# Kernel optimization log

Hardware: AMD Instinct MI355X
Metric: run time of the kernel (lower is better)

## Reference

```python
import jax, jax.numpy as jnp
import numpy as np
import math

N_NODES = 100000
N_EDGES = 3200000
F_IN = 512
HID = 128
N_CLS = 16


def setup_inputs() -> dict:
    key = jax.random.key(0)
    k = jax.random.split(key, 6)
    x = jax.random.normal(k[0], (N_NODES, F_IN), dtype=jnp.float32)
    edge_index = jax.random.randint(k[1], (2, N_EDGES), 0, N_NODES, dtype=jnp.int32)
    W1 = jax.random.normal(k[2], (F_IN, HID), dtype=jnp.float32) / np.sqrt(F_IN)
    W2 = jax.random.normal(k[3], (HID, HID), dtype=jnp.float32) / np.sqrt(HID)
    W3 = jax.random.normal(k[4], (N_CLS, HID), dtype=jnp.float32) / np.sqrt(HID)
    b3 = jnp.zeros((N_CLS,), dtype=jnp.float32)
    return {"x": x, "edge_index": edge_index, "W1": W1, "W2": W2, "W3": W3, "b3": b3}


def _sym_norm(edge_index, num_nodes, dtype):
    # add self loops with fill_value = trunc(log2(average_node_degree))
    E = edge_index.shape[1]
    fill = float(math.trunc(math.log2(E / num_nodes)))
    loops = jnp.arange(num_nodes, dtype=edge_index.dtype)
    row = jnp.concatenate([edge_index[0], loops])
    col = jnp.concatenate([edge_index[1], loops])
    w = jnp.concatenate([jnp.ones((E,), dtype), jnp.full((num_nodes,), fill, dtype)])
    deg = jax.ops.segment_sum(w, row, num_segments=num_nodes)
    deg_inv_sqrt = jnp.where(deg > 0, jax.lax.rsqrt(deg), 0.0)
    norm = deg_inv_sqrt[row] * w * deg_inv_sqrt[col]
    return row, col, norm


def reference(x, edge_index, W1, W2, W3, b3):
    N = x.shape[0]
    row, col, norm = _sym_norm(edge_index, N, x.dtype)

    def gcn(h, W):
        h = h @ W                                   # [N, d_out]
        msg = norm[:, None] * h[col]                # gather + scale, [E', d_out]
        return jax.ops.segment_sum(msg, row, num_segments=N)

    h = jax.nn.relu(gcn(x, W1))      # layer 1 + srelu (threshold clamped at 0)
    h = gcn(h, W2)                   # layer 2
    # dropout p=0.5 is identity in eval mode
    return h @ W3.T + b3             # linear classifier [N, n_classes]
```

## Files before the change

### kernel.cpp

```cpp
#include <hip/hip_runtime.h>
#include <cmath>

typedef __attribute__((ext_vector_type(8))) short short8;
typedef __attribute__((ext_vector_type(8))) unsigned short ushort8;
typedef __attribute__((ext_vector_type(4))) float f32x4;
typedef __attribute__((ext_vector_type(2))) float f32x2;
typedef __attribute__((ext_vector_type(4))) unsigned int uint4v;
typedef __attribute__((ext_vector_type(2))) int int2v;

#define EPB 4096
#define BCAP 20480

__device__ inline float bf16_lo(unsigned int p) {
  union { unsigned int i; float f; } v; v.i = p << 16; return v.f;
}
__device__ inline float bf16_hi(unsigned int p) {
  union { unsigned int i; float f; } v; v.i = p & 0xffff0000u; return v.f;
}
__device__ inline f32x2 bf2(unsigned int p) {
  union { unsigned int i; float f; } lo, hi;
  lo.i = p << 16;
  hi.i = p & 0xffff0000u;
  return (f32x2){lo.f, hi.f};
}
__device__ inline float bf16u(unsigned short w) {
  union { unsigned int i; float f; } v; v.i = (unsigned int)w << 16; return v.f;
}
__device__ inline unsigned short f32_to_bf16(float f) {
  union { float f; unsigned int i; } v; v.f = f;
  unsigned int x = v.i;
  x += 0x7fffu + ((x >> 16) & 1u);
  return (unsigned short)(x >> 16);
}

__global__ __launch_bounds__(256) void bin_k(const int* __restrict__ rows,
                                             const int* __restrict__ cols,
                                             int* __restrict__ bucket_cursor,
                                             unsigned int* __restrict__ binned, int E) {
  __shared__ int lhist[256];
  __shared__ int gbase[256];
  __shared__ int loff[256];
  const int t = threadIdx.x;
  const int base = blockIdx.x * EPB;
  lhist[t] = 0;
  __syncthreads();

  int bk[16];
  unsigned int pk[16];
#pragma unroll
  for (int j = 0; j < 16; ++j) {
    int e = base + j * 256 + t;
    if (e < E) {
      int r = rows[e];
      int c = cols[e];
      bk[j] = r >> 9;
      pk[j] = ((unsigned int)(r & 511) << 17) | (unsigned int)c;
      atomicAdd(&lhist[bk[j]], 1);
    } else {
      bk[j] = -1;
    }
  }
  __syncthreads();
  if (lhist[t] > 0) gbase[t] = atomicAdd(&bucket_cursor[t], lhist[t]);
  loff[t] = 0;
  __syncthreads();
#pragma unroll
  for (int j = 0; j < 16; ++j) {
    if (bk[j] >= 0) {
      int rank = gbase[bk[j]] + atomicAdd(&loff[bk[j]], 1);
      if (rank < BCAP) binned[(size_t)bk[j] * BCAP + rank] = pk[j];
    }
  }
}

__global__ __launch_bounds__(1024) void bucket_csr_k(const unsigned int* __restrict__ binned,
                                                     const int* __restrict__ bucket_cursor,
                                                     int2v* __restrict__ rowse,
                                                     float* __restrict__ dis,
                                                     int* __restrict__ col_sorted,
                                                     int N, float fill) {
  __shared__ int lcnt[512];
  __shared__ int lscan[512];
  const int b = blockIdx.x;
  const int t = threadIdx.x;
  const int start = b * BCAP;
  int cnt = bucket_cursor[b];
  if (cnt > BCAP) cnt = BCAP;
  const int endb = start + cnt;
  const int rbase = b << 9;

  if (t < 512) lcnt[t] = 0;
  __syncthreads();
  for (int i = start + t; i < endb; i += 1024)
    atomicAdd(&lcnt[binned[i] >> 17], 1);
  __syncthreads();

  int v = (t < 512) ? lcnt[t] : 0;
  if (t < 512) lscan[t] = v;
  __syncthreads();
  for (int off = 1; off < 512; off <<= 1) {
    int add = (t < 512 && t >= off) ? lscan[t - off] : 0;
    __syncthreads();
    if (t < 512) lscan[t] += add;
    __syncthreads();
  }

  if (t < 512) {
    int excl = lscan[t] - v;
    int r = rbase + t;
    if (r < N) {
      rowse[r] = (int2v){start + excl, start + excl + v};
      float d = (float)v + fill;
      dis[r] = d > 0.f ? rsqrtf(d) : 0.f;
    }
    lcnt[t] = excl;
  }
  __syncthreads();

  for (int i = start + t; i < endb; i += 1024) {
    unsigned int pk = binned[i];
    int rl = (int)(pk >> 17);
    int c = (int)(pk & 0x1FFFFu);
    int pos = atomicAdd(&lcnt[rl], 1);
    col_sorted[start + pos] = c;
  }
}

__global__ __launch_bounds__(256) void cast_w_k(const float* __restrict__ W1,
                                                const float* __restrict__ W2,
                                                const float* __restrict__ W3,
                                                unsigned short* __restrict__ W1t,
                                                unsigned short* __restrict__ W2t,
                                                unsigned short* __restrict__ W3b,
                                                int FIN) {
  int g = blockIdx.x * 256 + threadIdx.x;
  int n1 = FIN * 128;
  if (g < n1) {
    int n = g & 127, k = g >> 7;
    W1t[n * FIN + k] = f32_to_bf16(W1[(size_t)k * 128 + n]);
  } else if (g < n1 + 128 * 128) {
    int gg = g - n1;
    int n = gg & 127, k = gg >> 7;
    W2t[n * 128 + k] = f32_to_bf16(W2[k * 128 + n]);
  } else if (g < n1 + 128 * 128 + 16 * 128) {
    int gg = g - n1 - 128 * 128;
    W3b[gg] = f32_to_bf16(W3[gg]);
  }
}

__global__ __launch_bounds__(256) void gemm_k(const void* __restrict__ Aq, int a_is_f32,
                                              int M, int K,
                                              const unsigned short* __restrict__ Bt,
                                              const float* __restrict__ dis,
                                              unsigned short* __restrict__ C) {
  __shared__ unsigned short Al[64 * 40];
  __shared__ unsigned short Bl[128 * 40];
  const int t = threadIdx.x;
  const int bm = blockIdx.x * 64;
  const int lane = t & 63;
  const int wave = t >> 6;
  const int wm = (wave >> 1) * 32;
  const int wn = (wave & 1) * 64;
  const int l15 = lane & 15;
  const int l4 = lane >> 4;

  f32x4 acc[2][4];
#pragma unroll
  for (int a = 0; a < 2; ++a)
#pragma unroll
    for (int b = 0; b < 4; ++b) acc[a][b] = (f32x4){0.f, 0.f, 0.f, 0.f};

  const int am = t >> 2;
  const int ak = (t & 3) * 8;
  const int bn = t >> 1;
  const int bk = (t & 1) * 16;
  const int arow = bm + am;
  const bool arow_ok = arow < M;

  auto load_a = [&](int k0) -> ushort8 {
    ushort8 av = {0, 0, 0, 0, 0, 0, 0, 0};
    if (a_is_f32) {
      const float* A = (const float*)Aq;
      if (arow_ok) {
        const float* p = A + (size_t)arow * K + k0 + ak;
#pragma unroll
        for (int j = 0; j < 8; ++j) av[j] = f32_to_bf16(p[j]);
      }
    } else {
      const unsigned short* A = (const unsigned short*)Aq;
      if (arow_ok) av = *(const ushort8*)(A + (size_t)arow * K + k0 + ak);
    }
    return av;
  };

  ushort8 av = load_a(0);
  ushort8 bv0 = *(const ushort8*)(Bt + (size_t)bn * K + bk);
  ushort8 bv1 = *(const ushort8*)(Bt + (size_t)bn * K + bk + 8);

  for (int k0 = 0; k0 < K; k0 += 32) {
    *(ushort8*)&Al[am * 40 + ak] = av;
    *(ushort8*)&Bl[bn * 40 + bk] = bv0;
    *(ushort8*)&Bl[bn * 40 + bk + 8] = bv1;
    __syncthreads();

    const int kn = k0 + 32;
    if (kn < K) {
      av = load_a(kn);
      bv0 = *(const ushort8*)(Bt + (size_t)bn * K + kn + bk);
      bv1 = *(const ushort8*)(Bt + (size_t)bn * K + kn + bk + 8);
    }

    short8 a0 = *(const short8*)&Al[(wm + l15) * 40 + l4 * 8];
    short8 a1 = *(const short8*)&Al[(wm + 16 + l15) * 40 + l4 * 8];
#pragma unroll
    for (int nt = 0; nt < 4; ++nt) {
      short8 bfr = *(const short8*)&Bl[(wn + nt * 16 + l15) * 40 + l4 * 8];
      acc[0][nt] = __builtin_amdgcn_mfma_f32_16x16x32_bf16(a0, bfr, acc[0][nt], 0, 0, 0);
      acc[1][nt] = __builtin_amdgcn_mfma_f32_16x16x32_bf16(a1, bfr, acc[1][nt], 0, 0, 0);
    }
    __syncthreads();
  }

#pragma unroll
  for (int mt = 0; mt < 2; ++mt) {
    int rbase = bm + wm + mt * 16 + l4 * 4;
#pragma unroll
    for (int r = 0; r < 4; ++r) {
      int row = rbase + r;
      if (row < M) {
        float dr = dis[row];
#pragma unroll
        for (int nt = 0; nt < 4; ++nt) {
          int col = wn + nt * 16 + l15;
          C[(size_t)row * 128 + col] = f32_to_bf16(acc[mt][nt][r] * dr);
        }
      }
    }
  }
}

__global__ __launch_bounds__(256) void agg_k(const unsigned short* __restrict__ hs,
                                             const int2v* __restrict__ rowse,
                                             const int* __restrict__ cols,
                                             const float* __restrict__ dis,
                                             unsigned short* __restrict__ out_bf,
                                             const unsigned short* __restrict__ W3b,
                                             const float* __restrict__ b3,
                                             float* __restrict__ fcout,
                                             int N, float fill, int mode) {
  int r = blockIdx.x * 4 + (threadIdx.x >> 6);
  if (r >= N) return;
  const int lane = threadIdx.x & 63;
  const int sub = lane >> 4;
  const int fl = lane & 15;
  const uint4v* hv = (const uint4v*)hs;

  f32x2 a4[4];
#pragma unroll
  for (int k = 0; k < 4; ++k) a4[k] = (f32x2){0.f, 0.f};

  int2v se = rowse[r];
  int e = se.x;
  const int end = se.y;

  for (; e + 32 <= end; e += 32) {
    unsigned int c0 = (unsigned int)cols[e + sub];
    unsigned int c1 = (unsigned int)cols[e + 4 + sub];
    unsigned int c2 = (unsigned int)cols[e + 8 + sub];
    unsigned int c3 = (unsigned int)cols[e + 12 + sub];
    unsigned int c4 = (unsigned int)cols[e + 16 + sub];
    unsigned int c5 = (unsigned int)cols[e + 20 + sub];
    unsigned int c6 = (unsigned int)cols[e + 24 + sub];
    unsigned int c7 = (unsigned int)cols[e + 28 + sub];
    uint4v p0 = hv[c0 * 16u + fl];
    uint4v p1 = hv[c1 * 16u + fl];
    uint4v p2 = hv[c2 * 16u + fl];
    uint4v p3 = hv[c3 * 16u + fl];
    uint4v p4 = hv[c4 * 16u + fl];
    uint4v p5 = hv[c5 * 16u + fl];
    uint4v p6 = hv[c6 * 16u + fl];
    uint4v p7 = hv[c7 * 16u + fl];
#pragma unroll
    for (int k = 0; k < 4; ++k) {
      f32x2 s0 = (bf2(p0[k]) + bf2(p1[k])) + (bf2(p2[k]) + bf2(p3[k]));
      f32x2 s1 = (bf2(p4[k]) + bf2(p5[k])) + (bf2(p6[k]) + bf2(p7[k]));
      a4[k] += s0 + s1;
    }
  }
  for (; e + 8 <= end; e += 8) {
    unsigned int c0 = (unsigned int)cols[e + sub];
    unsigned int c1 = (unsigned int)cols[e + 4 + sub];
    uint4v p0 = hv[c0 * 16u + fl];
    uint4v p1 = hv[c1 * 16u + fl];
#pragma unroll
    for (int k = 0; k < 4; ++k) a4[k] += bf2(p0[k]) + bf2(p1[k]);
  }
  for (; e < end; e += 4) {
    int ee = e + sub;
    bool ok = ee < end;
    unsigned int c = ok ? (unsigned int)cols[ee] : (unsigned int)r;
    uint4v p = hv[c * 16u + fl];
    if (!ok) p = (uint4v){0, 0, 0, 0};
#pragma unroll
    for (int k = 0; k < 4; ++k) a4[k] += bf2(p[k]);
  }

#pragma unroll
  for (int k = 0; k < 4; ++k) {
    a4[k].x += __shfl_xor(a4[k].x, 16);
    a4[k].y += __shfl_xor(a4[k].y, 16);
    a4[k].x += __shfl_xor(a4[k].x, 32);
    a4[k].y += __shfl_xor(a4[k].y, 32);
  }

  if (sub == 0) {
    uint4v ps = hv[(unsigned int)r * 16u + fl];
    float dr = dis[r];
    float v[8];
#pragma unroll
    for (int k = 0; k < 4; ++k) {
      v[2 * k]     = dr * (a4[k].x + fill * bf16_lo(ps[k]));
      v[2 * k + 1] = dr * (a4[k].y + fill * bf16_hi(ps[k]));
    }
    if (mode == 0) {
      uint4v o;
#pragma unroll
      for (int k = 0; k < 4; ++k) {
        float f0 = fmaxf(v[2 * k], 0.f);
        float f1 = fmaxf(v[2 * k + 1], 0.f);
        o[k] = ((unsigned int)f32_to_bf16(f1) << 16) | (unsigned int)f32_to_bf16(f0);
      }
      *((uint4v*)out_bf + (unsigned int)r * 16u + fl) = o;
    } else {
      float p[16];
#pragma unroll
      for (int c = 0; c < 16; ++c) {
        ushort8 wr = *(const ushort8*)(W3b + c * 128 + fl * 8);
        float s = v[0] * bf16u(wr[0]);
        s = fmaf(v[1], bf16u(wr[1]), s);
        s = fmaf(v[2], bf16u(wr[2]), s);
        s = fmaf(v[3], bf16u(wr[3]), s);
        s = fmaf(v[4], bf16u(wr[4]), s);
        s = fmaf(v[5], bf16u(wr[5]), s);
        s = fmaf(v[6], bf16u(wr[6]), s);
        s = fmaf(v[7], bf16u(wr[7]), s);
        p[c] = s;
      }
#pragma unroll
      for (int m = 1; m <= 8; m <<= 1)
#pragma unroll
        for (int c = 0; c < 16; ++c) p[c] += __shfl_xor(p[c], m);
      fcout[(size_t)r * 16 + fl] = p[fl] + b3[fl];
    }
  }
}

extern "C" void kernel_launch(void* const* d_in, const int* in_sizes, int n_in,
                              void* d_out, int out_size, void* d_ws, size_t ws_size,
                              hipStream_t stream) {
  const float* x  = (const float*)d_in[0];
  const int* edge = (const int*)d_in[1];
  const float* W1 = (const float*)d_in[2];
  const float* W2 = (const float*)d_in[3];
  const float* W3 = (const float*)d_in[4];
  const float* b3 = (const float*)d_in[5];
  float* out = (float*)d_out;

  const int HID = 128;
  const int FIN = in_sizes[2] / HID;
  const int N   = in_sizes[0] / FIN;
  const int E   = in_sizes[1] / 2;
  const float fill = truncf(log2f((float)E / (float)N));

  char* w = (char*)d_ws;
  size_t off = 0;
  auto alloc = [&](size_t bytes) -> void* {
    void* p = w + off;
    off += (bytes + 255) & ~(size_t)255;
    return p;
  };
  const int NB = (N + 511) >> 9;
  float* dis      = (float*)alloc((size_t)N * 4);
  int2v* rowse    = (int2v*)alloc((size_t)N * 8);
  int* col_sorted = (int*)alloc((size_t)NB * BCAP * 4);
  int* bucket_cursor = (int*)alloc(256 * 4);
  unsigned int* binned = (unsigned int*)alloc((size_t)NB * BCAP * 4);
  unsigned short* W1t  = (unsigned short*)alloc((size_t)FIN * 128 * 2);
  unsigned short* W2t  = (unsigned short*)alloc(128 * 128 * 2);
  unsigned short* W3b  = (unsigned short*)alloc(16 * 128 * 2);
  unsigned short* bufA = (unsigned short*)alloc((size_t)N * 128 * 2);
  unsigned short* bufB = (unsigned short*)alloc((size_t)N * 128 * 2);

  const int* rows  = edge;
  const int* colsp = edge + E;

  hipMemsetAsync(bucket_cursor, 0, 256 * 4, stream);
  bin_k<<<(E + EPB - 1) / EPB, 256, 0, stream>>>(rows, colsp, bucket_cursor, binned, E);
  bucket_csr_k<<<NB, 1024, 0, stream>>>(binned, bucket_cursor, rowse, dis,
                                        col_sorted, N, fill);
  const int castN = FIN * 128 + 128 * 128 + 16 * 128;
  cast_w_k<<<(castN + 255) / 256, 256, 0, stream>>>(W1, W2, W3, W1t, W2t, W3b, FIN);

  const int gm = (N + 63) / 64;
  gemm_k<<<gm, 256, 0, stream>>>(x, 1, N, FIN, W1t, dis, bufA);
  agg_k<<<(N + 3) / 4, 256, 0, stream>>>(bufA, rowse, col_sorted, dis, bufB,
                                         W3b, b3, out, N, fill, 0);
  gemm_k<<<gm, 256, 0, stream>>>(bufB, 0, N, HID, W2t, dis, bufA);
  agg_k<<<(N + 3) / 4, 256, 0, stream>>>(bufA, rowse, col_sorted, dis, bufB,
                                         W3b, b3, out, N, fill, 1);
}
```

Baseline: 651.6 us.

## Map one 16-lane group per row with degree-sorted row permutation in aggregation

```diff
diff --git a/kernel.cpp b/kernel.cpp
--- a/kernel.cpp
+++ b/kernel.cpp
@@ -31,6 +31,11 @@
   unsigned int x = v.i;
   x += 0x7fffu + ((x >> 16) & 1u);
   return (unsigned short)(x >> 16);
+}
+__device__ inline f32x2 pk_add(f32x2 a, f32x2 b) {
+  f32x2 d;
+  asm("v_pk_add_f32 %0, %1, %2" : "=v"(d) : "v"(a), "v"(b));
+  return d;
 }
 
 __global__ __launch_bounds__(256) void bin_k(const int* __restrict__ rows,
@@ -78,9 +83,12 @@
                                                      int2v* __restrict__ rowse,
                                                      float* __restrict__ dis,
                                                      int* __restrict__ col_sorted,
+                                                     int* __restrict__ perm,
                                                      int N, float fill) {
   __shared__ int lcnt[512];
   __shared__ int lscan[512];
+  __shared__ int dh[512];
+  __shared__ int ds2[512];
   const int b = blockIdx.x;
   const int t = threadIdx.x;
   const int start = b * BCAP;
@@ -114,6 +122,32 @@
       dis[r] = d > 0.f ? rsqrtf(d) : 0.f;
     }
     lcnt[t] = excl;
+  }
+
+  if (t < 512) dh[t] = 0;
+  __syncthreads();
+  int key = 0;
+  if (t < 512) {
+    key = 511 - (v < 511 ? v : 511);
+    atomicAdd(&dh[key], 1);
+  }
+  __syncthreads();
+  if (t < 512) ds2[t] = dh[t];
+  __syncthreads();
+  for (int off = 1; off < 512; off <<= 1) {
+    int add = (t < 512 && t >= off) ? ds2[t - off] : 0;
+    __syncthreads();
+    if (t < 512) ds2[t] += add;
+    __syncthreads();
+  }
+  int base2 = 0;
+  if (t < 512) base2 = ds2[t] - dh[t];
+  __syncthreads();
+  if (t < 512) dh[t] = base2;
+  __syncthreads();
+  if (t < 512) {
+    int rank = atomicAdd(&dh[key], 1);
+    perm[(b << 9) + rank] = rbase + t;
   }
   __syncthreads();
 
@@ -243,115 +277,91 @@
                                              const int2v* __restrict__ rowse,
                                              const int* __restrict__ cols,
                                              const float* __restrict__ dis,
+                                             const int* __restrict__ perm,
                                              unsigned short* __restrict__ out_bf,
                                              const unsigned short* __restrict__ W3b,
                                              const float* __restrict__ b3,
                                              float* __restrict__ fcout,
                                              int N, float fill, int mode) {
-  int r = blockIdx.x * 4 + (threadIdx.x >> 6);
-  if (r >= N) return;
-  const int lane = threadIdx.x & 63;
-  const int sub = lane >> 4;
-  const int fl = lane & 15;
-  const uint4v* hv = (const uint4v*)hs;
-
-  f32x2 a4[4];
-#pragma unroll
-  for (int k = 0; k < 4; ++k) a4[k] = (f32x2){0.f, 0.f};
-
-  int2v se = rowse[r];
+  const int q = blockIdx.x * 16 + (threadIdx.x >> 4);
+  const unsigned int fl = threadIdx.x & 15;
+  const int rid = perm[q];
+  if (rid >= N) return;
+  const char* __restrict__ hsc = (const char*)hs;
+  const unsigned int flo = fl << 4;
+
+  int2v se = rowse[rid];
   int e = se.x;
   const int end = se.y;
 
-  for (; e + 32 <= end; e += 32) {
-    unsigned int c0 = (unsigned int)cols[e + sub];
-    unsigned int c1 = (unsigned int)cols[e + 4 + sub];
-    unsigned int c2 = (unsigned int)cols[e + 8 + sub];
-    unsigned int c3 = (unsigned int)cols[e + 12 + sub];
-    unsigned int c4 = (unsigned int)cols[e + 16 + sub];
-    unsigned int c5 = (unsigned int)cols[e + 20 + sub];
-    unsigned int c6 = (unsigned int)cols[e + 24 + sub];
-    unsigned int c7 = (unsigned int)cols[e + 28 + sub];
-    uint4v p0 = hv[c0 * 16u + fl];
-    uint4v p1 = hv[c1 * 16u + fl];
-    uint4v p2 = hv[c2 * 16u + fl];
-    uint4v p3 = hv[c3 * 16u + fl];
-    uint4v p4 = hv[c4 * 16u + fl];
-    uint4v p5 = hv[c5 * 16u + fl];
-    uint4v p6 = hv[c6 * 16u + fl];
-    uint4v p7 = hv[c7 * 16u + fl];
+  f32x2 a0 = {0.f, 0.f}, a1 = {0.f, 0.f}, a2 = {0.f, 0.f}, a3 = {0.f, 0.f};
+
+  for (; e + 4 <= end; e += 4) {
+    unsigned int c0 = (unsigned int)cols[e];
+    unsigned int c1 = (unsigned int)cols[e + 1];
+    unsigned int c2 = (unsigned int)cols[e + 2];
+    unsigned int c3 = (unsigned int)cols[e + 3];
+    uint4v p0 = *(const uint4v*)(hsc + ((c0 << 8) | flo));
+    uint4v p1 = *(const uint4v*)(hsc + ((c1 << 8) | flo));
+    uint4v p2 = *(const uint4v*)(hsc + ((c2 << 8) | flo));
+    uint4v p3 = *(const uint4v*)(hsc + ((c3 << 8) | flo));
+    a0 = pk_add(a0, bf2(p0[0])); a1 = pk_add(a1, bf2(p0[1]));
+    a2 = pk_add(a2, bf2(p0[2])); a3 = pk_add(a3, bf2(p0[3]));
+    a0 = pk_add(a0, bf2(p1[0])); a1 = pk_add(a1, bf2(p1[1]));
+    a2 = pk_add(a2, bf2(p1[2])); a3 = pk_add(a3, bf2(p1[3]));
+    a0 = pk_add(a0, bf2(p2[0])); a1 = pk_add(a1, bf2(p2[1]));
+    a2 = pk_add(a2, bf2(p2[2])); a3 = pk_add(a3, bf2(p2[3]));
+    a0 = pk_add(a0, bf2(p3[0])); a1 = pk_add(a1, bf2(p3[1]));
+    a2 = pk_add(a2, bf2(p3[2])); a3 = pk_add(a3, bf2(p3[3]));
+  }
+  for (; e < end; ++e) {
+    unsigned int c = (unsigned int)cols[e];
+    uint4v p = *(const uint4v*)(hsc + ((c << 8) | flo));
+    a0 = pk_add(a0, bf2(p[0])); a1 = pk_add(a1, bf2(p[1]));
+    a2 = pk_add(a2, bf2(p[2])); a3 = pk_add(a3, bf2(p[3]));
+  }
+
+  uint4v ps = *(const uint4v*)(hsc + (((unsigned int)rid << 8) | flo));
+  float dr = dis[rid];
+  float v[8];
+  v[0] = dr * (a0.x + fill * bf16_lo(ps[0]));
+  v[1] = dr * (a0.y + fill * bf16_hi(ps[0]));
+  v[2] = dr * (a1.x + fill * bf16_lo(ps[1]));
+  v[3] = dr * (a1.y + fill * bf16_hi(ps[1]));
+  v[4] = dr * (a2.x + fill * bf16_lo(ps[2]));
+  v[5] = dr * (a2.y + fill * bf16_hi(ps[2]));
+  v[6] = dr * (a3.x + fill * bf16_lo(ps[3]));
+  v[7] = dr * (a3.y + fill * bf16_hi(ps[3]));
+
+  if (mode == 0) {
+    uint4v o;
 #pragma unroll
     for (int k = 0; k < 4; ++k) {
-      f32x2 s0 = (bf2(p0[k]) + bf2(p1[k])) + (bf2(p2[k]) + bf2(p3[k]));
-      f32x2 s1 = (bf2(p4[k]) + bf2(p5[k])) + (bf2(p6[k]) + bf2(p7[k]));
-      a4[k] += s0 + s1;
-    }
-  }
-  for (; e + 8 <= end; e += 8) {
-    unsigned int c0 = (unsigned int)cols[e + sub];
-    unsigned int c1 = (unsigned int)cols[e + 4 + sub];
-    uint4v p0 = hv[c0 * 16u + fl];
-    uint4v p1 = hv[c1 * 16u + fl];
-#pragma unroll
-    for (int k = 0; k < 4; ++k) a4[k] += bf2(p0[k]) + bf2(p1[k]);
-  }
-  for (; e < end; e += 4) {
-    int ee = e + sub;
-    bool ok = ee < end;
-    unsigned int c = ok ? (unsigned int)cols[ee] : (unsigned int)r;
-    uint4v p = hv[c * 16u + fl];
-    if (!ok) p = (uint4v){0, 0, 0, 0};
-#pragma unroll
-    for (int k = 0; k < 4; ++k) a4[k] += bf2(p[k]);
-  }
-
-#pragma unroll
-  for (int k = 0; k < 4; ++k) {
-    a4[k].x += __shfl_xor(a4[k].x, 16);
-    a4[k].y += __shfl_xor(a4[k].y, 16);
-    a4[k].x += __shfl_xor(a4[k].x, 32);
-    a4[k].y += __shfl_xor(a4[k].y, 32);
-  }
-
-  if (sub == 0) {
-    uint4v ps = hv[(unsigned int)r * 16u + fl];
-    float dr = dis[r];
-    float v[8];
-#pragma unroll
-    for (int k = 0; k < 4; ++k) {
-      v[2 * k]     = dr * (a4[k].x + fill * bf16_lo(ps[k]));
-      v[2 * k + 1] = dr * (a4[k].y + fill * bf16_hi(ps[k]));
-    }
-    if (mode == 0) {
-      uint4v o;
-#pragma unroll
-      for (int k = 0; k < 4; ++k) {
-        float f0 = fmaxf(v[2 * k], 0.f);
-        float f1 = fmaxf(v[2 * k + 1], 0.f);
-        o[k] = ((unsigned int)f32_to_bf16(f1) << 16) | (unsigned int)f32_to_bf16(f0);
-      }
-      *((uint4v*)out_bf + (unsigned int)r * 16u + fl) = o;
-    } else {
-      float p[16];
-#pragma unroll
-      for (int c = 0; c < 16; ++c) {
-        ushort8 wr = *(const ushort8*)(W3b + c * 128 + fl * 8);
-        float s = v[0] * bf16u(wr[0]);
-        s = fmaf(v[1], bf16u(wr[1]), s);
-        s = fmaf(v[2], bf16u(wr[2]), s);
-        s = fmaf(v[3], bf16u(wr[3]), s);
-        s = fmaf(v[4], bf16u(wr[4]), s);
-        s = fmaf(v[5], bf16u(wr[5]), s);
-        s = fmaf(v[6], bf16u(wr[6]), s);
-        s = fmaf(v[7], bf16u(wr[7]), s);
-        p[c] = s;
-      }
-#pragma unroll
-      for (int m = 1; m <= 8; m <<= 1)
-#pragma unroll
-        for (int c = 0; c < 16; ++c) p[c] += __shfl_xor(p[c], m);
-      fcout[(size_t)r * 16 + fl] = p[fl] + b3[fl];
-    }
+      float f0 = fmaxf(v[2 * k], 0.f);
+      float f1 = fmaxf(v[2 * k + 1], 0.f);
+      o[k] = ((unsigned int)f32_to_bf16(f1) << 16) | (unsigned int)f32_to_bf16(f0);
+    }
+    *(uint4v*)((char*)out_bf + (((unsigned int)rid << 8) | flo)) = o;
+  } else {
+    float p[16];
+#pragma unroll
+    for (int c = 0; c < 16; ++c) {
+      ushort8 wr = *(const ushort8*)(W3b + c * 128 + fl * 8);
+      float s = v[0] * bf16u(wr[0]);
+      s = fmaf(v[1], bf16u(wr[1]), s);
+      s = fmaf(v[2], bf16u(wr[2]), s);
+      s = fmaf(v[3], bf16u(wr[3]), s);
+      s = fmaf(v[4], bf16u(wr[4]), s);
+      s = fmaf(v[5], bf16u(wr[5]), s);
+      s = fmaf(v[6], bf16u(wr[6]), s);
+      s = fmaf(v[7], bf16u(wr[7]), s);
+      p[c] = s;
+    }
+#pragma unroll
+    for (int m = 1; m <= 8; m <<= 1)
+#pragma unroll
+      for (int c = 0; c < 16; ++c) p[c] += __shfl_xor(p[c], m);
+    fcout[(size_t)rid * 16 + fl] = p[fl] + b3[fl];
   }
 }
 
@@ -382,6 +392,7 @@
   const int NB = (N + 511) >> 9;
   float* dis      = (float*)alloc((size_t)N * 4);
   int2v* rowse    = (int2v*)alloc((size_t)N * 8);
+  int* perm       = (int*)alloc((size_t)NB * 512 * 4);
   int* col_sorted = (int*)alloc((size_t)NB * BCAP * 4);
   int* bucket_cursor = (int*)alloc(256 * 4);
   unsigned int* binned = (unsigned int*)alloc((size_t)NB * BCAP * 4);
@@ -397,15 +408,15 @@
   hipMemsetAsync(bucket_cursor, 0, 256 * 4, stream);
   bin_k<<<(E + EPB - 1) / EPB, 256, 0, stream>>>(rows, colsp, bucket_cursor, binned, E);
   bucket_csr_k<<<NB, 1024, 0, stream>>>(binned, bucket_cursor, rowse, dis,
-                                        col_sorted, N, fill);
+                                        col_sorted, perm, N, fill);
   const int castN = FIN * 128 + 128 * 128 + 16 * 128;
   cast_w_k<<<(castN + 255) / 256, 256, 0, stream>>>(W1, W2, W3, W1t, W2t, W3b, FIN);
 
   const int gm = (N + 63) / 64;
   gemm_k<<<gm, 256, 0, stream>>>(x, 1, N, FIN, W1t, dis, bufA);
-  agg_k<<<(N + 3) / 4, 256, 0, stream>>>(bufA, rowse, col_sorted, dis, bufB,
-                                         W3b, b3, out, N, fill, 0);
+  agg_k<<<NB * 32, 256, 0, stream>>>(bufA, rowse, col_sorted, dis, perm, bufB,
+                                     W3b, b3, out, N, fill, 0);
   gemm_k<<<gm, 256, 0, stream>>>(bufB, 0, N, HID, W2t, dis, bufA);
-  agg_k<<<(N + 3) / 4, 256, 0, stream>>>(bufA, rowse, col_sorted, dis, bufB,
-                                         W3b, b3, out, N, fill, 1);
-}
+  agg_k<<<NB * 32, 256, 0, stream>>>(bufA, rowse, col_sorted, dis, perm, bufB,
+                                     W3b, b3, out, N, fill, 1);
+}
```

New measurement: 643.1 us. No clear change (-1.3%).
